# Kernel optimization log

Hardware: AMD Instinct MI355X
Metric: run time of the kernel (lower is better)

Reference implementation:

```python
import math
import jax, jax.numpy as jnp
import numpy as np

N, L, W = 64, 128, 256          # batch, num windows, window size
D, H, NL = 384, 8, 4            # d_model, heads, transformer layers
DFF = 1536
CH = [1, 4, 16, 64]             # conv channels (multiplier 4)
K = 7                            # conv kernel, pad 3, stride 1; pool k2 s2
LIN_IN = 64 * 32                # cnn_linear_size = 2048


def _pe(l, d):
    pos = np.arange(l)[:, None].astype(np.float32)
    i = np.arange(d // 2)[None, :].astype(np.float32)
    ang = pos / np.power(10000.0, 2.0 * i / d)
    pe = np.zeros((l, d), np.float32)
    pe[:, 0::2] = np.sin(ang)
    pe[:, 1::2] = np.cos(ang)
    return jnp.asarray(pe)


def _conv1d(x, w, b):
    y = jax.lax.conv_general_dilated(x, w, window_strides=(1,), padding=[(3, 3)],
                                     dimension_numbers=('NCH', 'OIH', 'NCH'))
    return y + b[None, :, None]


def _maxpool2(x):
    return jax.lax.reduce_window(x, -jnp.inf, jax.lax.max, (1, 1, 2), (1, 1, 2), 'VALID')


def _ln(x, g, b):
    m = x.mean(-1, keepdims=True)
    v = ((x - m) ** 2).mean(-1, keepdims=True)
    return (x - m) * jax.lax.rsqrt(v + 1e-5) * g + b


def setup_inputs() -> dict:
    key = jax.random.key(0)
    ks = iter(jax.random.split(key, 40))
    s = 0.02
    d = {'x': jax.random.normal(next(ks), (N, L, W), jnp.float32)}
    for i in range(3):
        d[f'conv_w{i}'] = jax.random.normal(next(ks), (CH[i + 1], CH[i], K), jnp.float32) * s
        d[f'conv_b{i}'] = jnp.zeros((CH[i + 1],), jnp.float32)
    d['embed_w'] = jax.random.normal(next(ks), (LIN_IN, D), jnp.float32) * s
    d['embed_b'] = jnp.zeros((D,), jnp.float32)
    for nm, sh in [('Wq', (NL, D, D)), ('Wk', (NL, D, D)), ('Wv', (NL, D, D)), ('Wo', (NL, D, D)),
                   ('W1', (NL, D, DFF)), ('W2', (NL, DFF, D))]:
        d[nm] = jax.random.normal(next(ks), sh, jnp.float32) * s
    for nm, sh in [('bq', (NL, D)), ('bk', (NL, D)), ('bv', (NL, D)), ('bo', (NL, D)),
                   ('b1', (NL, DFF)), ('b2', (NL, D))]:
        d[nm] = jnp.zeros(sh, jnp.float32)
    d['g1'] = jnp.ones((NL, D), jnp.float32); d['be1'] = jnp.zeros((NL, D), jnp.float32)
    d['g2'] = jnp.ones((NL, D), jnp.float32); d['be2'] = jnp.zeros((NL, D), jnp.float32)
    d['cls_w'] = jax.random.normal(next(ks), (D, 1), jnp.float32) * s
    d['cls_b'] = jnp.zeros((1,), jnp.float32)
    return d


def reference(x, conv_w0, conv_b0, conv_w1, conv_b1, conv_w2, conv_b2,
              embed_w, embed_b, Wq, bq, Wk, bk, Wv, bv, Wo, bo,
              W1, b1, W2, b2, g1, be1, g2, be2, cls_w, cls_b):
    n, l, w = x.shape
    # ---- CNN window encoder: each window -> d_model token ----
    h = x.reshape(n * l, 1, w)
    for cw, cb in ((conv_w0, conv_b0), (conv_w1, conv_b1), (conv_w2, conv_b2)):
        h = _maxpool2(jax.nn.relu(_conv1d(h, cw, cb)))
    h = h.reshape(n * l, -1)                      # (N*L, cnn_linear_size)
    h = jax.nn.relu(h @ embed_w + embed_b)        # (N*L, D)
    t = h.reshape(n, l, D) + _pe(l, D)
    # ---- transformer encoder (fast_transformers post-norm layers) ----
    E = D // H
    temp = 1.0 / math.sqrt(E)
    for i in range(Wq.shape[0]):
        q = (t @ Wq[i] + bq[i]).reshape(n, l, H, E)
        k = (t @ Wk[i] + bk[i]).reshape(n, l, H, E)
        v = (t @ Wv[i] + bv[i]).reshape(n, l, H, E)
        A = jax.nn.softmax(temp * jnp.einsum('nlhe,nshe->nhls', q, k), axis=-1)
        o = jnp.einsum('nhls,nshd->nlhd', A, v).reshape(n, l, D)
        t = _ln(t + o @ Wo[i] + bo[i], g1[i], be1[i])
        y = jax.nn.relu(t @ W1[i] + b1[i]) @ W2[i] + b2[i]
        t = _ln(t + y, g2[i], be2[i])
    # ---- classifier head: mean pool over windows -> logit ----
    return t.mean(axis=1) @ cls_w + cls_b          # (N, 1)
```

## Files before the change

### kernel.cpp

```cpp
#include <hip/hip_runtime.h>
#include <math.h>


typedef float f32x4 __attribute__((ext_vector_type(4)));
typedef short bf16x8 __attribute__((ext_vector_type(8)));
typedef short s16x4 __attribute__((ext_vector_type(4)));

__device__ __forceinline__ short f2bf(float f) {
    union { float f; unsigned u; } c; c.f = f;
    unsigned r = (c.u + 0x7FFFu + ((c.u >> 16) & 1u)) >> 16;
    return (short)r;
}
__device__ __forceinline__ float bf2f(short s) {
    union { unsigned u; float f; } c;
    c.u = ((unsigned)(unsigned short)s) << 16;
    return c.f;
}

__device__ __forceinline__ void gload_lds16(const void* g, void* l) {
    __builtin_amdgcn_global_load_lds(
        (const __attribute__((address_space(1))) unsigned int*)g,
        (__attribute__((address_space(3))) unsigned int*)l,
        16, 0, 0);
}

__global__ __launch_bounds__(256) void prep_kernel(
    const float* __restrict__ ew,
    const float* __restrict__ Wq, const float* __restrict__ Wk,
    const float* __restrict__ Wv, const float* __restrict__ Wo,
    const float* __restrict__ W1, const float* __restrict__ W2,
    const float* __restrict__ bq, const float* __restrict__ bk,
    const float* __restrict__ bv, const float* __restrict__ w2,
    short* __restrict__ ewT, short* __restrict__ WqkvT,
    short* __restrict__ WoT, short* __restrict__ W1T,
    short* __restrict__ W2T, float* __restrict__ pe,
    float* __restrict__ bqkv, short* __restrict__ w2T)
{
    __shared__ float tile[32][33];
    int id = blockIdx.x;
    int tid = threadIdx.x;
    int tx = tid & 31, ty = tid >> 5;

    const float* Wp;
    short* Wtp;
    int K, N, kb, nb;

    if (id < 768) {
        K = 2048; N = 384;
        kb = (id & 63) * 32; nb = (id >> 6) * 32;
        Wp = ew; Wtp = ewT;
    } else if (id < 2496) {
        int t = id - 768;
        int kbi = t % 12, nbi = (t / 12) % 12, z = t / 144;
        int layer = z / 3, which = z - layer * 3;
        K = 384; N = 384; kb = kbi * 32; nb = nbi * 32;
        Wp = (which == 0 ? Wq : (which == 1 ? Wk : Wv)) + (size_t)layer * 147456;
        Wtp = WqkvT + (size_t)layer * 442368 + (size_t)which * 147456;
    } else if (id < 3072) {
        int t = id - 2496;
        int kbi = t % 12, nbi = (t / 12) % 12, z = t / 144;
        K = 384; N = 384; kb = kbi * 32; nb = nbi * 32;
        Wp = Wo + (size_t)z * 147456; Wtp = WoT + (size_t)z * 147456;
    } else if (id < 5376) {
        int t = id - 3072;
        int kbi = t % 12, nbi = (t / 12) % 48, z = t / 576;
        K = 384; N = 1536; kb = kbi * 32; nb = nbi * 32;
        Wp = W1 + (size_t)z * 589824; Wtp = W1T + (size_t)z * 589824;
    } else if (id < 7680) {
        int t = id - 5376;
        int kbi = t % 48, nbi = (t / 48) % 12, z = t / 576;
        K = 1536; N = 384; kb = kbi * 32; nb = nbi * 32;
        Wp = W2 + (size_t)z * 589824; Wtp = W2T + (size_t)z * 589824;
    } else if (id < 7872) {
        int idx = (id - 7680) * 256 + tid;
        int l = idx / 384, d = idx - l * 384;
        int i2 = d >> 1;
        float ang = (float)l * expf(-(2.0f * (float)i2 / 384.0f) * 9.210340371976184f);
        pe[idx] = (d & 1) ? cosf(ang) : sinf(ang);
        return;
    } else if (id < 7890) {
        int idx = (id - 7872) * 256 + tid;
        int l = idx / 1152, j3 = idx - l * 1152;
        int which = j3 / 384, j = j3 - which * 384;
        const float* b = (which == 0 ? bq : (which == 1 ? bk : bv));
        bqkv[idx] = b[l * 384 + j];
        return;
    } else {
        int idx = (id - 7890) * 256 + tid;
        int c = idx >> 7, r = idx & 127;
        int pr = r >> 5, q = (r >> 3) & 3, j = r & 7;
        int ci = (q & 1) * 8 + j;
        int sft = 2 * pr + (q >> 1);
        w2T[idx] = (sft < 7) ? f2bf(w2[c * 112 + ci * 7 + sft]) : (short)0;
        return;
    }

    #pragma unroll
    for (int r = ty; r < 32; r += 8)
        tile[r][tx] = Wp[(size_t)(kb + r) * N + nb + tx];
    __syncthreads();
    #pragma unroll
    for (int r = ty; r < 32; r += 8)
        Wtp[(size_t)(nb + r) * K + kb + tx] = f2bf(tile[tx][r]);
}

__global__ __launch_bounds__(256, 4) void cnn_kernel(
    const float* __restrict__ x,
    const float* __restrict__ w0, const float* __restrict__ b0,
    const float* __restrict__ w1, const float* __restrict__ b1,
    const short* __restrict__ w2T, const float* __restrict__ b2,
    short* __restrict__ feat)
{
    __shared__ __align__(16) char smem[26880];
    float* xs  = (float*)smem;
    float* p0  = (float*)(smem + 4224);
    short* p1T = (short*)(smem + 13056);

    int tid = threadIdx.x;
    int w = tid >> 6, lane = tid & 63;
    size_t win = (size_t)blockIdx.x * 4 + w;
    int cq = lane >> 4, cl = lane & 15;

    float* xs_w = xs + w * 264;
    float* p0_w = p0 + w * 552;
    short* p1T_w = p1T + w * 1728;

    int ca = lane & 3;
    int cb = lane & 15, g = lane >> 4;
    float w0r[7], w1r[4][7];
    float b0r = b0[ca];
    float b1r = b1[cb];
    #pragma unroll
    for (int k = 0; k < 7; ++k) w0r[k] = w0[ca * 7 + k];
    #pragma unroll
    for (int ci = 0; ci < 4; ++ci)
        #pragma unroll
        for (int k = 0; k < 7; ++k) w1r[ci][k] = w1[(cb * 4 + ci) * 7 + k];

    {
        f32x4 v = *(const f32x4*)(x + win * 256 + lane * 4);
        *(f32x4*)&xs_w[4 + lane * 4] = v;
        if (lane < 2) *(f32x4*)&xs_w[lane * 260] = (f32x4){0.f, 0.f, 0.f, 0.f};
    }

    {
        int pa = lane >> 2;
        #pragma unroll
        for (int t2 = 0; t2 < 8; ++t2) {
            int pp = t2 * 16 + pa;
            float rv[9];
            #pragma unroll
            for (int u = 0; u < 9; ++u) rv[u] = xs_w[2 * pp + u + 1];
            float a0 = b0r, a1 = b0r;
            #pragma unroll
            for (int k = 0; k < 7; ++k) {
                a0 = fmaf(w0r[k], rv[k], a0);
                a1 = fmaf(w0r[k], rv[k + 1], a1);
            }
            p0_w[ca * 138 + pp + 3] = fmaxf(fmaxf(a0, a1), 0.f);
        }
        if (lane < 4) {
            p0_w[lane * 138 + 0] = 0.f;
            p0_w[lane * 138 + 1] = 0.f;
            p0_w[lane * 138 + 2] = 0.f;
            p0_w[lane * 138 + 131] = 0.f;
            p0_w[lane * 138 + 132] = 0.f;
            p0_w[lane * 138 + 133] = 0.f;
        }
    }

    #pragma unroll
    for (int cc = 0; cc < 4; ++cc) {
        int cci = (cc + g) & 3;
        int j0 = g * 32 + cci * 8;
        float acc[8];
        #pragma unroll
        for (int m = 0; m < 8; ++m) acc[m] = b1r;
        #pragma unroll
        for (int ci = 0; ci < 4; ++ci) {
            float rv[14];
            #pragma unroll
            for (int u = 0; u < 14; ++u) rv[u] = p0_w[ci * 138 + j0 + u];
            #pragma unroll
            for (int k = 0; k < 7; ++k) {
                float ww = w1r[ci][k];
                #pragma unroll
                for (int m = 0; m < 8; ++m) acc[m] = fmaf(ww, rv[m + k], acc[m]);
            }
        }
        int po = g * 16 + cci * 4;
        #pragma unroll
        for (int m = 0; m < 4; ++m)
            p1T_w[(3 + po + m) * 24 + cb] =
                f2bf(fmaxf(fmaxf(acc[2 * m], acc[2 * m + 1]), 0.f));
    }
    {
        int* pz = (int*)p1T_w;
        if (lane < 36) pz[lane] = 0;
        if (lane < 60) pz[804 + lane] = 0;
    }
    __syncthreads();

    f32x4 acc[4][4];
    #pragma unroll
    for (int v = 0; v < 4; ++v)
        #pragma unroll
        for (int mt = 0; mt < 4; ++mt)
            acc[v][mt] = (f32x4){0.f, 0.f, 0.f, 0.f};

    {
        const short* bpb = p1T + (w * 16 + cl + (cq >> 1)) * 24 + (cq & 1) * 8;
        #pragma unroll
        for (int pr = 0; pr < 4; ++pr) {
            bf16x8 bfr[4];
            #pragma unroll
            for (int v = 0; v < 4; ++v)
                bfr[v] = *(const bf16x8*)&bpb[v * 1728 + pr * 48];
            #pragma unroll
            for (int mt = 0; mt < 4; ++mt) {
                bf16x8 af = *(const bf16x8*)&w2T[(mt * 16 + cl) * 128 +
                                                 pr * 32 + cq * 8];
                #pragma unroll
                for (int v = 0; v < 4; ++v)
                    acc[v][mt] = __builtin_amdgcn_mfma_f32_16x16x32_bf16(
                        af, bfr[v], acc[v][mt], 0, 0, 0);
            }
        }
    }

    int iev = (w * 16 + cl) >> 1;
    #pragma unroll
    for (int v = 0; v < 4; ++v) {
        short* fp = feat + ((size_t)blockIdx.x * 4 + v) * 2048;
        #pragma unroll
        for (int mt = 0; mt < 4; ++mt) {
            #pragma unroll
            for (int rg = 0; rg < 4; ++rg) {
                float vv = acc[v][mt][rg];
                float v2 = __shfl_xor(vv, 1, 64);
                if ((cl & 1) == 0) {
                    int c = mt * 16 + cq * 4 + rg;
                    float pv = fmaxf(fmaxf(vv, v2) + b2[c], 0.f);
                    fp[c * 32 + iev] = f2bf(pv);
                }
            }
        }
    }
}

template <int EPI>
__global__ __launch_bounds__(256) void gemm_bf16(
    const short* __restrict__ A, const short* __restrict__ Bt,
    const float* __restrict__ bias, const float* __restrict__ resid,
    const float* __restrict__ pe, float* __restrict__ outF,
    short* __restrict__ outB, int M, int N, int K)
{
    __shared__ short As[2][128 * 64];
    __shared__ short Bs[2][64 * 64];
    int tid = threadIdx.x;
    int w = tid >> 6, lane = tid & 63;
    int wm = w >> 1, wn = w & 1;
    int m0 = blockIdx.y * 128, n0 = blockIdx.x * 64;

    int rl = lane >> 3, sl = lane & 7;
    int cb = sl ^ rl;
    const short* aptr[4];
    const short* bptr[2];
    int arow[4], brow[2];
    #pragma unroll
    for (int l = 0; l < 4; ++l) {
        arow[l] = l * 32 + w * 8;
        aptr[l] = A + (size_t)(m0 + arow[l] + rl) * K + cb * 8;
    }
    #pragma unroll
    for (int l = 0; l < 2; ++l) {
        brow[l] = l * 32 + w * 8;
        bptr[l] = Bt + (size_t)(n0 + brow[l] + rl) * K + cb * 8;
    }

    int cq = lane >> 4, cl = lane & 15;
    f32x4 acc[4][2];
    #pragma unroll
    for (int mt = 0; mt < 4; ++mt)
        #pragma unroll
        for (int nt = 0; nt < 2; ++nt)
            acc[mt][nt] = (f32x4){0.f, 0.f, 0.f, 0.f};

    #pragma unroll
    for (int l = 0; l < 4; ++l) { gload_lds16(aptr[l], &As[0][arow[l] * 64]); aptr[l] += 64; }
    #pragma unroll
    for (int l = 0; l < 2; ++l) { gload_lds16(bptr[l], &Bs[0][brow[l] * 64]); bptr[l] += 64; }
    __syncthreads();

    int nk = K >> 6;
    for (int k = 0; k < nk; ++k) {
        int cur = k & 1;
        if (k + 1 < nk) {
            #pragma unroll
            for (int l = 0; l < 4; ++l) { gload_lds16(aptr[l], &As[cur ^ 1][arow[l] * 64]); aptr[l] += 64; }
            #pragma unroll
            for (int l = 0; l < 2; ++l) { gload_lds16(bptr[l], &Bs[cur ^ 1][brow[l] * 64]); bptr[l] += 64; }
        }
        #pragma unroll
        for (int s = 0; s < 2; ++s) {
            bf16x8 afr[4], bfr[2];
            #pragma unroll
            for (int mt = 0; mt < 4; ++mt) {
                int r = wm * 64 + mt * 16 + cl;
                int slot = (s * 4 + cq) ^ (r & 7);
                afr[mt] = *(const bf16x8*)&As[cur][r * 64 + slot * 8];
            }
            #pragma unroll
            for (int nt = 0; nt < 2; ++nt) {
                int r = wn * 32 + nt * 16 + cl;
                int slot = (s * 4 + cq) ^ (r & 7);
                bfr[nt] = *(const bf16x8*)&Bs[cur][r * 64 + slot * 8];
            }
            #pragma unroll
            for (int mt = 0; mt < 4; ++mt)
                #pragma unroll
                for (int nt = 0; nt < 2; ++nt)
                    acc[mt][nt] = __builtin_amdgcn_mfma_f32_16x16x32_bf16(
                        afr[mt], bfr[nt], acc[mt][nt], 0, 0, 0);
        }
        __syncthreads();
    }

    #pragma unroll
    for (int mt = 0; mt < 4; ++mt) {
        #pragma unroll
        for (int nt = 0; nt < 2; ++nt) {
            int col = n0 + wn * 32 + nt * 16 + cl;
            float bb = bias[col];
            #pragma unroll
            for (int rg = 0; rg < 4; ++rg) {
                int row = m0 + wm * 64 + mt * 16 + cq * 4 + rg;
                float v = acc[mt][nt][rg] + bb;
                if (EPI & 1) v = fmaxf(v, 0.f);
                if (EPI & 4) v += pe[(row & 127) * 384 + col];
                if (EPI & 2) v += resid[(size_t)row * N + col];
                if (EPI & 8) outF[(size_t)row * N + col] = v;
                if (EPI & 16) outB[(size_t)row * N + col] = f2bf(v);
            }
        }
    }
}

template <int EPI>
__global__ __launch_bounds__(256) void gemm_bf16_wide(
    const short* __restrict__ A, const short* __restrict__ Bt,
    const float* __restrict__ bias, float* __restrict__ outF,
    short* __restrict__ outB, int M, int N, int K)
{
    __shared__ short As[2][128 * 32];
    __shared__ short Bs[2][128 * 32];
    int tid = threadIdx.x;
    int w = tid >> 6, lane = tid & 63;
    int wm = w >> 1, wn = w & 1;
    int m0 = blockIdx.y * 128, n0 = blockIdx.x * 128;

    int rl = lane >> 2, sl = lane & 3;
    int cb = sl ^ (rl & 3) ^ ((rl >> 2) & 3);
    const short* aptr[2];
    const short* bptr[2];
    int srow[2];
    #pragma unroll
    for (int l = 0; l < 2; ++l) {
        srow[l] = w * 32 + l * 16;
        aptr[l] = A + (size_t)(m0 + srow[l] + rl) * K + cb * 8;
        bptr[l] = Bt + (size_t)(n0 + srow[l] + rl) * K + cb * 8;
    }

    int cq = lane >> 4, cl = lane & 15;
    f32x4 acc[4][4];
    #pragma unroll
    for (int mt = 0; mt < 4; ++mt)
        #pragma unroll
        for (int nt = 0; nt < 4; ++nt)
            acc[mt][nt] = (f32x4){0.f, 0.f, 0.f, 0.f};

    #pragma unroll
    for (int l = 0; l < 2; ++l) {
        gload_lds16(aptr[l], &As[0][srow[l] * 32]);
        gload_lds16(bptr[l], &Bs[0][srow[l] * 32]);
        aptr[l] += 32; bptr[l] += 32;
    }
    __syncthreads();

    int nk = K >> 5;
    for (int k = 0; k < nk; ++k) {
        int cur = k & 1;
        if (k + 1 < nk) {
            #pragma unroll
            for (int l = 0; l < 2; ++l) {
                gload_lds16(aptr[l], &As[cur ^ 1][srow[l] * 32]);
                gload_lds16(bptr[l], &Bs[cur ^ 1][srow[l] * 32]);
                aptr[l] += 32; bptr[l] += 32;
            }
        }
        bf16x8 afr[4], bfr[4];
        #pragma unroll
        for (int mt = 0; mt < 4; ++mt) {
            int r = wm * 64 + mt * 16 + cl;
            int slot = cq ^ (r & 3) ^ ((r >> 2) & 3);
            afr[mt] = *(const bf16x8*)&As[cur][r * 32 + slot * 8];
        }
        #pragma unroll
        for (int nt = 0; nt < 4; ++nt) {
            int r = wn * 64 + nt * 16 + cl;
            int slot = cq ^ (r & 3) ^ ((r >> 2) & 3);
            bfr[nt] = *(const bf16x8*)&Bs[cur][r * 32 + slot * 8];
        }
        #pragma unroll
        for (int mt = 0; mt < 4; ++mt)
            #pragma unroll
            for (int nt = 0; nt < 4; ++nt)
                acc[mt][nt] = __builtin_amdgcn_mfma_f32_16x16x32_bf16(
                    afr[mt], bfr[nt], acc[mt][nt], 0, 0, 0);
        __syncthreads();
    }

    #pragma unroll
    for (int mt = 0; mt < 4; ++mt) {
        #pragma unroll
        for (int nt = 0; nt < 4; ++nt) {
            int col = n0 + wn * 64 + nt * 16 + cl;
            float bb = bias[col];
            #pragma unroll
            for (int rg = 0; rg < 4; ++rg) {
                int row = m0 + wm * 64 + mt * 16 + cq * 4 + rg;
                float v = acc[mt][nt][rg] + bb;
                if (EPI & 1) v = fmaxf(v, 0.f);
                if (EPI & 8) outF[(size_t)row * N + col] = v;
                if (EPI & 16) outB[(size_t)row * N + col] = f2bf(v);
            }
        }
    }
}

__global__ __launch_bounds__(512) void gemm_ln(
    const short* __restrict__ A, const short* __restrict__ Bt,
    const float* __restrict__ bias, const float* resid,
    const float* __restrict__ g, const float* __restrict__ be,
    float* t, short* __restrict__ tb, int K)
{
    __shared__ __align__(16) char smem[106496];
    short* As0 = (short*)smem;
    short* Bs0 = (short*)(smem + 8192);

    int tid = threadIdx.x;
    int w = tid >> 6, lane = tid & 63;
    int m0 = blockIdx.x * 32;
    int rl = lane >> 3, sl = lane & 7;
    int cb = sl ^ rl;

    const short* aptr = A + (size_t)(m0 + (w & 3) * 8 + rl) * K + cb * 8;
    const short* bptr[6];
    #pragma unroll
    for (int l = 0; l < 6; ++l)
        bptr[l] = Bt + (size_t)(w * 48 + l * 8 + rl) * K + cb * 8;

    int cq = lane >> 4, cl = lane & 15;
    f32x4 acc[2][3];
    #pragma unroll
    for (int mt = 0; mt < 2; ++mt)
        #pragma unroll
        for (int nt = 0; nt < 3; ++nt)
            acc[mt][nt] = (f32x4){0.f, 0.f, 0.f, 0.f};

    if (w < 4) { gload_lds16(aptr, &As0[(w * 8) * 64]); aptr += 64; }
    #pragma unroll
    for (int l = 0; l < 6; ++l) {
        gload_lds16(bptr[l], &Bs0[(w * 48 + l * 8) * 64]);
        bptr[l] += 64;
    }
    __syncthreads();

    int nk = K >> 6;
    for (int k = 0; k < nk; ++k) {
        int cur = k & 1;
        if (k + 1 < nk) {
            if (w < 4) { gload_lds16(aptr, &As0[(cur ^ 1) * 2048 + (w * 8) * 64]); aptr += 64; }
            #pragma unroll
            for (int l = 0; l < 6; ++l) {
                gload_lds16(bptr[l], &Bs0[(cur ^ 1) * 24576 + (w * 48 + l * 8) * 64]);
                bptr[l] += 64;
            }
        }
        const short* As = As0 + cur * 2048;
        const short* Bs = Bs0 + cur * 24576;
        #pragma unroll
        for (int s = 0; s < 2; ++s) {
            bf16x8 afr[2], bfr[3];
            #pragma unroll
            for (int mt = 0; mt < 2; ++mt) {
                int r = mt * 16 + cl;
                int slot = (s * 4 + cq) ^ (r & 7);
                afr[mt] = *(const bf16x8*)&As[r * 64 + slot * 8];
            }
            #pragma unroll
            for (int nt = 0; nt < 3; ++nt) {
                int r = w * 48 + nt * 16 + cl;
                int slot = (s * 4 + cq) ^ (r & 7);
                bfr[nt] = *(const bf16x8*)&Bs[r * 64 + slot * 8];
            }
            #pragma unroll
            for (int mt = 0; mt < 2; ++mt)
                #pragma unroll
                for (int nt = 0; nt < 3; ++nt)
                    acc[mt][nt] = __builtin_amdgcn_mfma_f32_16x16x32_bf16(
                        afr[mt], bfr[nt], acc[mt][nt], 0, 0, 0);
        }
        __syncthreads();
    }

    float* yb = (float*)smem;
    #pragma unroll
    for (int mt = 0; mt < 2; ++mt) {
        #pragma unroll
        for (int nt = 0; nt < 3; ++nt) {
            int col = w * 48 + nt * 16 + cl;
            float bb = bias[col];
            #pragma unroll
            for (int rg = 0; rg < 4; ++rg) {
                int rloc = mt * 16 + cq * 4 + rg;
                yb[rloc * 388 + col] =
                    acc[mt][nt][rg] + bb + resid[(size_t)(m0 + rloc) * 384 + col];
            }
        }
    }
    __syncthreads();

    int rloc = tid >> 4, sub = tid & 15;
    f32x4 vals[6];
    float s = 0.f, s2 = 0.f;
    #pragma unroll
    for (int m = 0; m < 6; ++m) {
        f32x4 vv = *(const f32x4*)&yb[rloc * 388 + m * 64 + sub * 4];
        vals[m] = vv;
        #pragma unroll
        for (int j = 0; j < 4; ++j) {
            s += vv[j];
            s2 = fmaf(vv[j], vv[j], s2);
        }
    }
    s += __shfl_xor(s, 1, 64);  s2 += __shfl_xor(s2, 1, 64);
    s += __shfl_xor(s, 2, 64);  s2 += __shfl_xor(s2, 2, 64);
    s += __shfl_xor(s, 4, 64);  s2 += __shfl_xor(s2, 4, 64);
    s += __shfl_xor(s, 8, 64);  s2 += __shfl_xor(s2, 8, 64);
    float mean = s * (1.f / 384.f);
    float var = s2 * (1.f / 384.f) - mean * mean;
    float inv = rsqrtf(var + 1e-5f);

    size_t ro = (size_t)(m0 + rloc) * 384;
    #pragma unroll
    for (int m = 0; m < 6; ++m) {
        int c0 = m * 64 + sub * 4;
        f32x4 gg = *(const f32x4*)&g[c0];
        f32x4 bb = *(const f32x4*)&be[c0];
        f32x4 ov;
        s16x4 ob2;
        #pragma unroll
        for (int j = 0; j < 4; ++j) {
            float v = (vals[m][j] - mean) * inv * gg[j] + bb[j];
            ov[j] = v;
            ob2[j] = f2bf(v);
        }
        *(f32x4*)&t[ro + c0] = ov;
        *(s16x4*)&tb[ro + c0] = ob2;
    }
}

__global__ __launch_bounds__(256) void qkvattn_kernel(
    const short* __restrict__ A, const short* __restrict__ Bt,
    const float* __restrict__ bias, short* __restrict__ o)
{
    __shared__ __align__(16) char smem[76544];
    short* As0 = (short*)smem;
    short* Bs0 = (short*)(smem + 32768);
    short* Qs  = (short*)smem;
    short* Ks  = (short*)(smem + 14336);
    short* Vt  = (short*)(smem + 28672);
    short* P   = (short*)(smem + 41728);

    int tid = threadIdx.x;
    int w = tid >> 6, lane = tid & 63;
    int cq = lane >> 4, cl = lane & 15;
    int n = blockIdx.x >> 3, h = blockIdx.x & 7;
    int m0 = n * 128;

    int rl = lane >> 3, sl = lane & 7;
    int cb = sl ^ rl;
    const short* aptr[4];
    int arow[4];
    #pragma unroll
    for (int l = 0; l < 4; ++l) {
        arow[l] = l * 32 + w * 8;
        aptr[l] = A + (size_t)(m0 + arow[l] + rl) * 384 + cb * 8;
    }
    const short* bptr[5];
    int brow[5];
    #pragma unroll
    for (int l = 0; l < 5; ++l) {
        brow[l] = (l < 4) ? (l * 32 + w * 8) : (128 + w * 8);
        int r = brow[l] + rl;
        int g0 = (r >= 96) ? 2 : ((r >= 48) ? 1 : 0);
        int loc = r - g0 * 48;
        bptr[l] = Bt + (size_t)(g0 * 384 + h * 48 + loc) * 384 + cb * 8;
    }

    f32x4 acc[2][9];
    #pragma unroll
    for (int mt = 0; mt < 2; ++mt)
        #pragma unroll
        for (int nt = 0; nt < 9; ++nt)
            acc[mt][nt] = (f32x4){0.f, 0.f, 0.f, 0.f};

    #pragma unroll
    for (int l = 0; l < 4; ++l) { gload_lds16(aptr[l], &As0[arow[l] * 64]); aptr[l] += 64; }
    #pragma unroll
    for (int l = 0; l < 5; ++l) {
        if (l < 4 || w < 2) { gload_lds16(bptr[l], &Bs0[brow[l] * 64]); }
        bptr[l] += 64;
    }
    __syncthreads();

    for (int k = 0; k < 6; ++k) {
        int cur = k & 1;
        if (k + 1 < 6) {
            #pragma unroll
            for (int l = 0; l < 4; ++l) {
                gload_lds16(aptr[l], &As0[(cur ^ 1) * 8192 + arow[l] * 64]);
                aptr[l] += 64;
            }
            #pragma unroll
            for (int l = 0; l < 5; ++l) {
                if (l < 4 || w < 2)
                    gload_lds16(bptr[l], &Bs0[(cur ^ 1) * 9216 + brow[l] * 64]);
                bptr[l] += 64;
            }
        }
        const short* Asb = As0 + cur * 8192;
        const short* Bsb = Bs0 + cur * 9216;
        #pragma unroll
        for (int s = 0; s < 2; ++s) {
            bf16x8 afr[2], bfr[9];
            #pragma unroll
            for (int mt = 0; mt < 2; ++mt) {
                int r = w * 32 + mt * 16 + cl;
                int slot = (s * 4 + cq) ^ (r & 7);
                afr[mt] = *(const bf16x8*)&Asb[r * 64 + slot * 8];
            }
            #pragma unroll
            for (int nt = 0; nt < 9; ++nt) {
                int r = nt * 16 + cl;
                int slot = (s * 4 + cq) ^ (r & 7);
                bfr[nt] = *(const bf16x8*)&Bsb[r * 64 + slot * 8];
            }
            #pragma unroll
            for (int mt = 0; mt < 2; ++mt)
                #pragma unroll
                for (int nt = 0; nt < 9; ++nt)
                    acc[mt][nt] = __builtin_amdgcn_mfma_f32_16x16x32_bf16(
                        afr[mt], bfr[nt], acc[mt][nt], 0, 0, 0);
        }
        __syncthreads();
    }

    const float* bh = bias + h * 48;
    #pragma unroll
    for (int mt = 0; mt < 2; ++mt) {
        #pragma unroll
        for (int nt = 0; nt < 9; ++nt) {
            int grp = nt / 3;
            int col = (nt - grp * 3) * 16 + cl;
            float bb = bh[grp * 384 + col];
            if (grp == 2) {
                int row0 = w * 32 + mt * 16 + cq * 4;
                s16x4 pv;
                #pragma unroll
                for (int rg = 0; rg < 4; ++rg) pv[rg] = f2bf(acc[mt][nt][rg] + bb);
                *(s16x4*)&Vt[col * 136 + row0] = pv;
            } else {
                short* dst = (grp == 0) ? Qs : Ks;
                #pragma unroll
                for (int rg = 0; rg < 4; ++rg) {
                    int row = w * 32 + mt * 16 + cq * 4 + rg;
                    dst[row * 56 + col] = f2bf(acc[mt][nt][rg] + bb);
                }
            }
        }
    }
    __syncthreads();

    const bf16x8 zf = (bf16x8){0, 0, 0, 0, 0, 0, 0, 0};
    bf16x8 qf[2][2];
    #pragma unroll
    for (int mt = 0; mt < 2; ++mt) {
        int r = w * 32 + mt * 16 + cl;
        qf[mt][0] = *(const bf16x8*)&Qs[r * 56 + cq * 8];
        qf[mt][1] = (cq < 2) ? *(const bf16x8*)&Qs[r * 56 + 32 + cq * 8] : zf;
    }

    f32x4 sacc[2][8];
    #pragma unroll
    for (int mt = 0; mt < 2; ++mt)
        #pragma unroll
        for (int kt = 0; kt < 8; ++kt)
            sacc[mt][kt] = (f32x4){0.f, 0.f, 0.f, 0.f};

    #pragma unroll
    for (int kt = 0; kt < 8; ++kt) {
        int r = kt * 16 + cl;
        bf16x8 kf0 = *(const bf16x8*)&Ks[r * 56 + cq * 8];
        bf16x8 kf1 = (cq < 2) ? *(const bf16x8*)&Ks[r * 56 + 32 + cq * 8] : zf;
        #pragma unroll
        for (int mt = 0; mt < 2; ++mt) {
            sacc[mt][kt] = __builtin_amdgcn_mfma_f32_16x16x32_bf16(
                qf[mt][0], kf0, sacc[mt][kt], 0, 0, 0);
            sacc[mt][kt] = __builtin_amdgcn_mfma_f32_16x16x32_bf16(
                qf[mt][1], kf1, sacc[mt][kt], 0, 0, 0);
        }
    }

    const float temp = 0.14433756729740643f;
    short* Pw = P + w * 4352;
    float denom[2][4];
    #pragma unroll
    for (int mt = 0; mt < 2; ++mt) {
        #pragma unroll
        for (int rg = 0; rg < 4; ++rg) {
            float mx = sacc[mt][0][rg];
            #pragma unroll
            for (int kt = 1; kt < 8; ++kt) mx = fmaxf(mx, sacc[mt][kt][rg]);
            mx = fmaxf(mx, __shfl_xor(mx, 1, 64));
            mx = fmaxf(mx, __shfl_xor(mx, 2, 64));
            mx = fmaxf(mx, __shfl_xor(mx, 4, 64));
            mx = fmaxf(mx, __shfl_xor(mx, 8, 64));
            int row = mt * 16 + cq * 4 + rg;
            float se = 0.f;
            #pragma unroll
            for (int kt = 0; kt < 8; ++kt) {
                float p = __expf(temp * (sacc[mt][kt][rg] - mx));
                se += p;
                Pw[row * 136 + kt * 16 + cl] = f2bf(p);
            }
            se += __shfl_xor(se, 1, 64);
            se += __shfl_xor(se, 2, 64);
            se += __shfl_xor(se, 4, 64);
            se += __shfl_xor(se, 8, 64);
            denom[mt][rg] = se;
        }
    }

    f32x4 oacc[2][3];
    #pragma unroll
    for (int mt = 0; mt < 2; ++mt)
        #pragma unroll
        for (int nt = 0; nt < 3; ++nt)
            oacc[mt][nt] = (f32x4){0.f, 0.f, 0.f, 0.f};

    #pragma unroll
    for (int ks = 0; ks < 4; ++ks) {
        bf16x8 paf[2];
        #pragma unroll
        for (int mt = 0; mt < 2; ++mt)
            paf[mt] = *(const bf16x8*)&Pw[(mt * 16 + cl) * 136 + ks * 32 + cq * 8];
        #pragma unroll
        for (int nt = 0; nt < 3; ++nt) {
            bf16x8 vf = *(const bf16x8*)&Vt[(nt * 16 + cl) * 136 + ks * 32 + cq * 8];
            #pragma unroll
            for (int mt = 0; mt < 2; ++mt)
                oacc[mt][nt] = __builtin_amdgcn_mfma_f32_16x16x32_bf16(
                    paf[mt], vf, oacc[mt][nt], 0, 0, 0);
        }
    }

    #pragma unroll
    for (int mt = 0; mt < 2; ++mt) {
        #pragma unroll
        for (int rg = 0; rg < 4; ++rg) {
            float inv = 1.f / denom[mt][rg];
            int qrow = w * 32 + mt * 16 + cq * 4 + rg;
            short* op = o + ((size_t)n * 128 + qrow) * 384 + h * 48;
            #pragma unroll
            for (int nt = 0; nt < 3; ++nt)
                op[nt * 16 + cl] = f2bf(oacc[mt][nt][rg] * inv);
        }
    }
}

__global__ __launch_bounds__(384) void head_kernel(
    const float* __restrict__ t, const float* __restrict__ cls_w,
    const float* __restrict__ cls_b, float* __restrict__ out)
{
    int n = blockIdx.x, d = threadIdx.x;
    float s = 0.f;
    for (int l = 0; l < 128; ++l) s += t[((size_t)n * 128 + l) * 384 + d];
    float p = s * (1.f / 128.f) * cls_w[d];
    #pragma unroll
    for (int off = 32; off > 0; off >>= 1) p += __shfl_xor(p, off, 64);
    __shared__ float red[6];
    if ((threadIdx.x & 63) == 0) red[threadIdx.x >> 6] = p;
    __syncthreads();
    if (threadIdx.x == 0) {
        float tot = red[0] + red[1] + red[2] + red[3] + red[4] + red[5];
        out[n] = tot + cls_b[0];
    }
}

extern "C" void kernel_launch(void* const* d_in, const int* in_sizes, int n_in,
                              void* d_out, int out_size, void* d_ws, size_t ws_size,
                              hipStream_t stream) {
    (void)n_in; (void)out_size; (void)ws_size;
    const float* x   = (const float*)d_in[0];
    const float* cw0 = (const float*)d_in[1];
    const float* cb0 = (const float*)d_in[2];
    const float* cw1 = (const float*)d_in[3];
    const float* cb1 = (const float*)d_in[4];
    const float* cw2 = (const float*)d_in[5];
    const float* cb2 = (const float*)d_in[6];
    const float* ew  = (const float*)d_in[7];
    const float* eb  = (const float*)d_in[8];
    bool dict_order = (in_sizes[10] == 589824);
    const float *Wq, *Wk, *Wv, *Wo, *W1, *W2, *bq, *bk, *bv, *bo, *b1, *b2;
    if (dict_order) {
        Wq = (const float*)d_in[9];  Wk = (const float*)d_in[10];
        Wv = (const float*)d_in[11]; Wo = (const float*)d_in[12];
        W1 = (const float*)d_in[13]; W2 = (const float*)d_in[14];
        bq = (const float*)d_in[15]; bk = (const float*)d_in[16];
        bv = (const float*)d_in[17]; bo = (const float*)d_in[18];
        b1 = (const float*)d_in[19]; b2 = (const float*)d_in[20];
    } else {
        Wq = (const float*)d_in[9];  bq = (const float*)d_in[10];
        Wk = (const float*)d_in[11]; bk = (const float*)d_in[12];
        Wv = (const float*)d_in[13]; bv = (const float*)d_in[14];
        Wo = (const float*)d_in[15]; bo = (const float*)d_in[16];
        W1 = (const float*)d_in[17]; b1 = (const float*)d_in[18];
        W2 = (const float*)d_in[19]; b2 = (const float*)d_in[20];
    }
    const float* g1  = (const float*)d_in[21];
    const float* be1 = (const float*)d_in[22];
    const float* g2  = (const float*)d_in[23];
    const float* be2 = (const float*)d_in[24];
    const float* clw = (const float*)d_in[25];
    const float* clb = (const float*)d_in[26];

    char* wp = (char*)d_ws;
    float* pe    = (float*)wp; wp += 196608;
    short* featb = (short*)wp; wp += 33554432;
    float* t     = (float*)wp; wp += 12582912;
    short* tb    = (short*)wp; wp += 6291456;
    short* qkvb  = (short*)wp; wp += 18874368;
    short* ob    = (short*)wp; wp += 6291456;
    short* ewT   = (short*)wp; wp += 1572864;
    short* WqkvT = (short*)wp; wp += 3538944;
    short* WoT   = (short*)wp; wp += 1179648;
    short* W1T   = (short*)wp; wp += 4718592;
    short* W2T   = (short*)wp; wp += 4718592;
    float* bqkv  = (float*)wp; wp += 18432;
    short* w2T   = (short*)wp; wp += 16384;
    short* hb    = featb;
    (void)qkvb;

    const int ROWS = 8192;

    prep_kernel<<<7922, 256, 0, stream>>>(ew, Wq, Wk, Wv, Wo, W1, W2,
                                          bq, bk, bv, cw2,
                                          ewT, WqkvT, WoT, W1T, W2T,
                                          pe, bqkv, w2T);
    cnn_kernel<<<2048, 256, 0, stream>>>(x, cw0, cb0, cw1, cb1, w2T, cb2, featb);

    gemm_bf16<29><<<dim3(6, 64), 256, 0, stream>>>(featb, ewT, eb, nullptr, pe,
                                                   t, tb, ROWS, 384, 2048);
    for (int i = 0; i < 4; ++i) {
        const short* WqkvTi = WqkvT + (size_t)i * 442368;
        const short* WoTi = WoT + (size_t)i * 147456;
        const short* W1Ti = W1T + (size_t)i * 589824;
        const short* W2Ti = W2T + (size_t)i * 589824;
        qkvattn_kernel<<<512, 256, 0, stream>>>(tb, WqkvTi, bqkv + i * 1152, ob);
        gemm_ln<<<256, 512, 0, stream>>>(ob, WoTi, bo + i * 384, t,
            g1 + i * 384, be1 + i * 384, t, tb, 384);
        gemm_bf16_wide<17><<<dim3(12, 64), 256, 0, stream>>>(tb, W1Ti,
            b1 + i * 1536, nullptr, hb, ROWS, 1536, 384);
        gemm_ln<<<256, 512, 0, stream>>>(hb, W2Ti, b2 + i * 384, t,
            g2 + i * 384, be2 + i * 384, t, tb, 1536);
    }
    head_kernel<<<64, 384, 0, stream>>>(t, clw, clb, (float*)d_out);
}
```

Measured before the change: 569.7 us.

## Fuse FFN up-projection, ReLU, down-projection and LayerNorm into one kernel

Replaces the separate W1 GEMM (writing the 8192x1536 bf16 hidden activation to global memory) and the W2 GEMM+LayerNorm with a single kernel. Each 32-row block computes 64-column hidden chunks in LDS and immediately accumulates them into the W2 output, then applies residual and LayerNorm. This removes the hidden-activation round trip through global memory and one launch per layer. In exchange each block re-streams all of W1 and W2 through LDS, has only 256 blocks, and computes just one MFMA tile per wave per chunk for the up-projection, which may limit MFMA utilisation and parallelism.

```diff
diff --git a/kernel.cpp b/kernel.cpp
--- a/kernel.cpp
+++ b/kernel.cpp
@@ -346,98 +346,6 @@
     }
 }
 
-template <int EPI>
-__global__ __launch_bounds__(256) void gemm_bf16_wide(
-    const short* __restrict__ A, const short* __restrict__ Bt,
-    const float* __restrict__ bias, float* __restrict__ outF,
-    short* __restrict__ outB, int M, int N, int K)
-{
-    __shared__ short As[2][128 * 32];
-    __shared__ short Bs[2][128 * 32];
-    int tid = threadIdx.x;
-    int w = tid >> 6, lane = tid & 63;
-    int wm = w >> 1, wn = w & 1;
-    int m0 = blockIdx.y * 128, n0 = blockIdx.x * 128;
-
-    int rl = lane >> 2, sl = lane & 3;
-    int cb = sl ^ (rl & 3) ^ ((rl >> 2) & 3);
-    const short* aptr[2];
-    const short* bptr[2];
-    int srow[2];
-    #pragma unroll
-    for (int l = 0; l < 2; ++l) {
-        srow[l] = w * 32 + l * 16;
-        aptr[l] = A + (size_t)(m0 + srow[l] + rl) * K + cb * 8;
-        bptr[l] = Bt + (size_t)(n0 + srow[l] + rl) * K + cb * 8;
-    }
-
-    int cq = lane >> 4, cl = lane & 15;
-    f32x4 acc[4][4];
-    #pragma unroll
-    for (int mt = 0; mt < 4; ++mt)
-        #pragma unroll
-        for (int nt = 0; nt < 4; ++nt)
-            acc[mt][nt] = (f32x4){0.f, 0.f, 0.f, 0.f};
-
-    #pragma unroll
-    for (int l = 0; l < 2; ++l) {
-        gload_lds16(aptr[l], &As[0][srow[l] * 32]);
-        gload_lds16(bptr[l], &Bs[0][srow[l] * 32]);
-        aptr[l] += 32; bptr[l] += 32;
-    }
-    __syncthreads();
-
-    int nk = K >> 5;
-    for (int k = 0; k < nk; ++k) {
-        int cur = k & 1;
-        if (k + 1 < nk) {
-            #pragma unroll
-            for (int l = 0; l < 2; ++l) {
-                gload_lds16(aptr[l], &As[cur ^ 1][srow[l] * 32]);
-                gload_lds16(bptr[l], &Bs[cur ^ 1][srow[l] * 32]);
-                aptr[l] += 32; bptr[l] += 32;
-            }
-        }
-        bf16x8 afr[4], bfr[4];
-        #pragma unroll
-        for (int mt = 0; mt < 4; ++mt) {
-            int r = wm * 64 + mt * 16 + cl;
-            int slot = cq ^ (r & 3) ^ ((r >> 2) & 3);
-            afr[mt] = *(const bf16x8*)&As[cur][r * 32 + slot * 8];
-        }
-        #pragma unroll
-        for (int nt = 0; nt < 4; ++nt) {
-            int r = wn * 64 + nt * 16 + cl;
-            int slot = cq ^ (r & 3) ^ ((r >> 2) & 3);
-            bfr[nt] = *(const bf16x8*)&Bs[cur][r * 32 + slot * 8];
-        }
-        #pragma unroll
-        for (int mt = 0; mt < 4; ++mt)
-            #pragma unroll
-            for (int nt = 0; nt < 4; ++nt)
-                acc[mt][nt] = __builtin_amdgcn_mfma_f32_16x16x32_bf16(
-                    afr[mt], bfr[nt], acc[mt][nt], 0, 0, 0);
-        __syncthreads();
-    }
-
-    #pragma unroll
-    for (int mt = 0; mt < 4; ++mt) {
-        #pragma unroll
-        for (int nt = 0; nt < 4; ++nt) {
-            int col = n0 + wn * 64 + nt * 16 + cl;
-            float bb = bias[col];
-            #pragma unroll
-            for (int rg = 0; rg < 4; ++rg) {
-                int row = m0 + wm * 64 + mt * 16 + cq * 4 + rg;
-                float v = acc[mt][nt][rg] + bb;
-                if (EPI & 1) v = fmaxf(v, 0.f);
-                if (EPI & 8) outF[(size_t)row * N + col] = v;
-                if (EPI & 16) outB[(size_t)row * N + col] = f2bf(v);
-            }
-        }
-    }
-}
-
 __global__ __launch_bounds__(512) void gemm_ln(
     const short* __restrict__ A, const short* __restrict__ Bt,
     const float* __restrict__ bias, const float* resid,
@@ -526,6 +434,170 @@
                 int rloc = mt * 16 + cq * 4 + rg;
                 yb[rloc * 388 + col] =
                     acc[mt][nt][rg] + bb + resid[(size_t)(m0 + rloc) * 384 + col];
+            }
+        }
+    }
+    __syncthreads();
+
+    int rloc = tid >> 4, sub = tid & 15;
+    f32x4 vals[6];
+    float s = 0.f, s2 = 0.f;
+    #pragma unroll
+    for (int m = 0; m < 6; ++m) {
+        f32x4 vv = *(const f32x4*)&yb[rloc * 388 + m * 64 + sub * 4];
+        vals[m] = vv;
+        #pragma unroll
+        for (int j = 0; j < 4; ++j) {
+            s += vv[j];
+            s2 = fmaf(vv[j], vv[j], s2);
+        }
+    }
+    s += __shfl_xor(s, 1, 64);  s2 += __shfl_xor(s2, 1, 64);
+    s += __shfl_xor(s, 2, 64);  s2 += __shfl_xor(s2, 2, 64);
+    s += __shfl_xor(s, 4, 64);  s2 += __shfl_xor(s2, 4, 64);
+    s += __shfl_xor(s, 8, 64);  s2 += __shfl_xor(s2, 8, 64);
+    float mean = s * (1.f / 384.f);
+    float var = s2 * (1.f / 384.f) - mean * mean;
+    float inv = rsqrtf(var + 1e-5f);
+
+    size_t ro = (size_t)(m0 + rloc) * 384;
+    #pragma unroll
+    for (int m = 0; m < 6; ++m) {
+        int c0 = m * 64 + sub * 4;
+        f32x4 gg = *(const f32x4*)&g[c0];
+        f32x4 bb = *(const f32x4*)&be[c0];
+        f32x4 ov;
+        s16x4 ob2;
+        #pragma unroll
+        for (int j = 0; j < 4; ++j) {
+            float v = (vals[m][j] - mean) * inv * gg[j] + bb[j];
+            ov[j] = v;
+            ob2[j] = f2bf(v);
+        }
+        *(f32x4*)&t[ro + c0] = ov;
+        *(s16x4*)&tb[ro + c0] = ob2;
+    }
+}
+
+__global__ __launch_bounds__(512) void ffn_ln(
+    const short* __restrict__ A,
+    const short* __restrict__ W1t,
+    const short* __restrict__ W2t,
+    const float* __restrict__ b1,
+    const float* __restrict__ bias2,
+    const float* resid,
+    const float* __restrict__ g, const float* __restrict__ be,
+    float* t, short* __restrict__ tb)
+{
+    __shared__ __align__(16) char smem[126976];
+    short* Ats = (short*)smem;
+    short* WsA = (short*)(smem + 24576);
+    short* WsB = (short*)(smem + 73728);
+    short* Hs  = (short*)(smem + 122880);
+
+    int tid = threadIdx.x;
+    int w = tid >> 6, lane = tid & 63;
+    int m0 = blockIdx.x * 32;
+    int rl = lane >> 3, sl = lane & 7;
+    int cb = sl ^ rl;
+    int cq = lane >> 4, cl = lane & 15;
+    int mt = w & 1, nth = w >> 1;
+
+    if (w < 4) {
+        #pragma unroll
+        for (int kc = 0; kc < 6; ++kc)
+            gload_lds16(A + (size_t)(m0 + w * 8 + rl) * 384 + kc * 64 + cb * 8,
+                        &Ats[(kc * 32 + w * 8) * 64]);
+    }
+    #pragma unroll
+    for (int kc = 0; kc < 6; ++kc)
+        gload_lds16(W1t + (size_t)(w * 8 + rl) * 384 + kc * 64 + cb * 8,
+                    &WsA[(kc * 64 + w * 8) * 64]);
+    __syncthreads();
+
+    f32x4 yacc[2][3];
+    #pragma unroll
+    for (int m2 = 0; m2 < 2; ++m2)
+        #pragma unroll
+        for (int nt = 0; nt < 3; ++nt)
+            yacc[m2][nt] = (f32x4){0.f, 0.f, 0.f, 0.f};
+
+    for (int c = 0; c < 24; ++c) {
+        #pragma unroll
+        for (int l = 0; l < 6; ++l)
+            gload_lds16(W2t + (size_t)(w * 48 + l * 8 + rl) * 1536 + c * 64 + cb * 8,
+                        &WsB[(w * 48 + l * 8) * 64]);
+
+        f32x4 hacc = (f32x4){0.f, 0.f, 0.f, 0.f};
+        #pragma unroll
+        for (int kc = 0; kc < 6; ++kc) {
+            #pragma unroll
+            for (int s = 0; s < 2; ++s) {
+                int ra = mt * 16 + cl;
+                int sa = (s * 4 + cq) ^ (ra & 7);
+                bf16x8 af = *(const bf16x8*)&Ats[(kc * 32 + ra) * 64 + sa * 8];
+                int rb = nth * 16 + cl;
+                int sb = (s * 4 + cq) ^ (rb & 7);
+                bf16x8 bf = *(const bf16x8*)&WsA[(kc * 64 + rb) * 64 + sb * 8];
+                hacc = __builtin_amdgcn_mfma_f32_16x16x32_bf16(af, bf, hacc, 0, 0, 0);
+            }
+        }
+        {
+            int lc = nth * 16 + cl;
+            float bb = b1[c * 64 + lc];
+            int sgrp = (lc >> 3);
+            #pragma unroll
+            for (int rg = 0; rg < 4; ++rg) {
+                int row = mt * 16 + cq * 4 + rg;
+                float v = fmaxf(hacc[rg] + bb, 0.f);
+                Hs[row * 64 + (sgrp ^ (row & 7)) * 8 + (lc & 7)] = f2bf(v);
+            }
+        }
+        __syncthreads();
+
+        if (c + 1 < 24) {
+            #pragma unroll
+            for (int kc = 0; kc < 6; ++kc)
+                gload_lds16(W1t + (size_t)((c + 1) * 64 + w * 8 + rl) * 384 + kc * 64 + cb * 8,
+                            &WsA[(kc * 64 + w * 8) * 64]);
+        }
+        #pragma unroll
+        for (int s = 0; s < 2; ++s) {
+            bf16x8 haf[2], wbf[3];
+            #pragma unroll
+            for (int m2 = 0; m2 < 2; ++m2) {
+                int r = m2 * 16 + cl;
+                int slot = (s * 4 + cq) ^ (r & 7);
+                haf[m2] = *(const bf16x8*)&Hs[r * 64 + slot * 8];
+            }
+            #pragma unroll
+            for (int nt = 0; nt < 3; ++nt) {
+                int r = w * 48 + nt * 16 + cl;
+                int slot = (s * 4 + cq) ^ (r & 7);
+                wbf[nt] = *(const bf16x8*)&WsB[r * 64 + slot * 8];
+            }
+            #pragma unroll
+            for (int m2 = 0; m2 < 2; ++m2)
+                #pragma unroll
+                for (int nt = 0; nt < 3; ++nt)
+                    yacc[m2][nt] = __builtin_amdgcn_mfma_f32_16x16x32_bf16(
+                        haf[m2], wbf[nt], yacc[m2][nt], 0, 0, 0);
+        }
+        __syncthreads();
+    }
+
+    float* yb = (float*)smem;
+    #pragma unroll
+    for (int m2 = 0; m2 < 2; ++m2) {
+        #pragma unroll
+        for (int nt = 0; nt < 3; ++nt) {
+            int col = w * 48 + nt * 16 + cl;
+            float bb = bias2[col];
+            #pragma unroll
+            for (int rg = 0; rg < 4; ++rg) {
+                int rloc = m2 * 16 + cq * 4 + rg;
+                yb[rloc * 388 + col] =
+                    yacc[m2][nt][rg] + bb + resid[(size_t)(m0 + rloc) * 384 + col];
             }
         }
     }
@@ -860,7 +932,6 @@
     short* W2T   = (short*)wp; wp += 4718592;
     float* bqkv  = (float*)wp; wp += 18432;
     short* w2T   = (short*)wp; wp += 16384;
-    short* hb    = featb;
     (void)qkvb;
 
     const int ROWS = 8192;
@@ -881,10 +952,8 @@
         qkvattn_kernel<<<512, 256, 0, stream>>>(tb, WqkvTi, bqkv + i * 1152, ob);
         gemm_ln<<<256, 512, 0, stream>>>(ob, WoTi, bo + i * 384, t,
             g1 + i * 384, be1 + i * 384, t, tb, 384);
-        gemm_bf16_wide<17><<<dim3(12, 64), 256, 0, stream>>>(tb, W1Ti,
-            b1 + i * 1536, nullptr, hb, ROWS, 1536, 384);
-        gemm_ln<<<256, 512, 0, stream>>>(hb, W2Ti, b2 + i * 384, t,
-            g2 + i * 384, be2 + i * 384, t, tb, 1536);
+        ffn_ln<<<256, 512, 0, stream>>>(tb, W1Ti, W2Ti, b1 + i * 1536,
+            b2 + i * 384, t, g2 + i * 384, be2 + i * 384, t, tb);
     }
     head_kernel<<<64, 384, 0, stream>>>(t, clw, clb, (float*)d_out);
 }
```

Result: no change. 573.5 us (+0.7%).
